# Optimization experiments

Hardware: AMD Instinct MI355X
Metric: run time of the kernel (lower is better)

## Reference

```python
import jax, jax.numpy as jnp
import numpy as np

N = 100000
H, C = 2, 16
EPS = 1e-16


def gatv2_conv(x, Wl, Wr, att, bias, src, dst, n):
    # x: [N, Fin]; Wl/Wr: [Fin, H*C]; att: [H, C]; bias: [H*C]
    xl = (x @ Wl).reshape(n, H, C)  # source-side transform
    xr = (x @ Wr).reshape(n, H, C)  # destination-side transform
    # per-edge GATv2 score: a^T LeakyReLU(xl_j + xr_i)
    z = jax.nn.leaky_relu(xl[src] + xr[dst], negative_slope=0.2)  # [E, H, C]
    e = jnp.einsum('ehc,hc->eh', z, att)  # [E, H]
    # softmax over incoming edges per destination node
    m = jax.ops.segment_max(e, dst, num_segments=n)  # [N, H]
    ex = jnp.exp(e - m[dst])
    s = jax.ops.segment_sum(ex, dst, num_segments=n)  # [N, H]
    alpha = ex / (s[dst] + EPS)  # [E, H]
    # scatter-add aggregation of weighted source features
    out = jax.ops.segment_sum(alpha[:, :, None] * xl[src], dst, num_segments=n)  # [N, H, C]
    return out.reshape(n, H * C) + bias


def setup_inputs() -> dict:
    key = jax.random.key(0)
    ks = jax.random.split(key, 12)
    F_in, n_cls, E = 1433, 7, 3200000
    x = jax.random.normal(ks[0], (N, F_in), dtype=jnp.float32)
    edge_index = jax.random.randint(ks[1], (2, E), 0, N, dtype=jnp.int64)
    sc = 0.05
    return {
        'x': x,
        'edge_index': edge_index,
        'Wl1': jax.random.normal(ks[2], (F_in, H * C), dtype=jnp.float32) * sc,
        'Wr1': jax.random.normal(ks[3], (F_in, H * C), dtype=jnp.float32) * sc,
        'a1': jax.random.normal(ks[4], (H, C), dtype=jnp.float32) * sc,
        'b1': jnp.zeros((H * C,), dtype=jnp.float32),
        'Wl2': jax.random.normal(ks[5], (H * C, H * C), dtype=jnp.float32) * sc,
        'Wr2': jax.random.normal(ks[6], (H * C, H * C), dtype=jnp.float32) * sc,
        'a2': jax.random.normal(ks[7], (H, C), dtype=jnp.float32) * sc,
        'b2': jnp.zeros((H * C,), dtype=jnp.float32),
        'fcW': jax.random.normal(ks[8], (H * C, n_cls), dtype=jnp.float32) * sc,
        'fcb': jnp.zeros((n_cls,), dtype=jnp.float32),
    }


def reference(x, edge_index, Wl1, Wr1, a1, b1, Wl2, Wr2, a2, b2, fcW, fcb):
    n = x.shape[0]
    loops = jnp.arange(n, dtype=edge_index.dtype)
    src = jnp.concatenate([edge_index[0], loops])  # add self-loops (PyG default)
    dst = jnp.concatenate([edge_index[1], loops])
    h = jax.nn.elu(gatv2_conv(x, Wl1, Wr1, a1, b1, src, dst, n))
    h = jax.nn.elu(gatv2_conv(h, Wl2, Wr2, a2, b2, src, dst, n))
    logits = h @ fcW + fcb
    return jax.nn.log_softmax(logits, axis=1)
```

## Files before the change

kernel.cpp:

```cpp
#include <hip/hip_runtime.h>
#include <hip/hip_bf16.h>
#include <cstddef>
#include <cstdint>

#define HC 32
#define NHEADS 2
#define CH 16
#define CAP 96

#define KK    1433
#define KFULL 1408
#define WTP   1440

typedef __bf16 bf16x8 __attribute__((ext_vector_type(8)));
typedef float  f32x4  __attribute__((ext_vector_type(4)));
typedef float  f32x4u __attribute__((ext_vector_type(4), aligned(4)));

#define BM 128

__global__ __launch_bounds__(256) void wprep(
    const float* __restrict__ Wl, const float* __restrict__ Wr,
    __bf16* __restrict__ Wt)
{
    int idx = blockIdx.x * 256 + threadIdx.x;
    if (idx >= 64 * WTP) return;
    int n = idx / WTP;
    int k = idx - n * WTP;
    float v = 0.f;
    if (k < KK) v = (n < HC) ? Wl[(size_t)k * HC + n]
                             : Wr[(size_t)k * HC + (n - HC)];
    Wt[idx] = (__bf16)v;
}

__global__ __launch_bounds__(256) void gemm_dual_mfma(
    const float* __restrict__ A, int N,
    const __bf16* __restrict__ Wt,
    float* __restrict__ XL, float* __restrict__ XR)
{
    const int tid  = threadIdx.x;
    const int lane = tid & 63;
    const int w    = tid >> 6;
    const int row0 = blockIdx.x * BM;
    const int frag_m = lane & 15;
    const int frag_k = lane >> 4;

    f32x4 acc[2][4];
    #pragma unroll
    for (int i = 0; i < 2; ++i)
        #pragma unroll
        for (int j = 0; j < 4; ++j) acc[i][j] = (f32x4){0.f, 0.f, 0.f, 0.f};

    int r0 = row0 + w * 32 + frag_m;
    int r1 = r0 + 16;
    int cr0 = (r0 < N) ? r0 : N - 1;
    int cr1 = (r1 < N) ? r1 : N - 1;
    const float* __restrict__ a0 = A + (size_t)cr0 * KK + frag_k * 8;
    const float* __restrict__ a1 = A + (size_t)cr1 * KK + frag_k * 8;
    const __bf16* __restrict__ wb = Wt + (size_t)frag_m * WTP + frag_k * 8;

    #pragma unroll 4
    for (int k0 = 0; k0 < KFULL; k0 += 32) {
        f32x4u u0 = *(const f32x4u*)(a0 + k0);
        f32x4u u1 = *(const f32x4u*)(a0 + k0 + 4);
        f32x4u v0 = *(const f32x4u*)(a1 + k0);
        f32x4u v1 = *(const f32x4u*)(a1 + k0 + 4);
        bf16x8 bfv[4];
        #pragma unroll
        for (int nt = 0; nt < 4; ++nt)
            bfv[nt] = *(const bf16x8*)(wb + (size_t)(nt * 16) * WTP + k0);
        bf16x8 af0, af1;
        #pragma unroll
        for (int j = 0; j < 4; ++j) {
            af0[j]     = (__bf16)u0[j];
            af0[j + 4] = (__bf16)u1[j];
            af1[j]     = (__bf16)v0[j];
            af1[j + 4] = (__bf16)v1[j];
        }
        #pragma unroll
        for (int nt = 0; nt < 4; ++nt) {
            acc[0][nt] = __builtin_amdgcn_mfma_f32_16x16x32_bf16(
                af0, bfv[nt], acc[0][nt], 0, 0, 0);
            acc[1][nt] = __builtin_amdgcn_mfma_f32_16x16x32_bf16(
                af1, bfv[nt], acc[1][nt], 0, 0, 0);
        }
    }

    {
        bf16x8 af0, af1, bfv[4];
        #pragma unroll
        for (int j = 0; j < 8; ++j) {
            int k = KFULL + frag_k * 8 + j;
            float x0 = (k < KK) ? a0[KFULL + j] : 0.f;
            float x1 = (k < KK) ? a1[KFULL + j] : 0.f;
            af0[j] = (__bf16)x0;
            af1[j] = (__bf16)x1;
        }
        #pragma unroll
        for (int nt = 0; nt < 4; ++nt)
            bfv[nt] = *(const bf16x8*)(wb + (size_t)(nt * 16) * WTP + KFULL);
        #pragma unroll
        for (int nt = 0; nt < 4; ++nt) {
            acc[0][nt] = __builtin_amdgcn_mfma_f32_16x16x32_bf16(
                af0, bfv[nt], acc[0][nt], 0, 0, 0);
            acc[1][nt] = __builtin_amdgcn_mfma_f32_16x16x32_bf16(
                af1, bfv[nt], acc[1][nt], 0, 0, 0);
        }
    }

    const int cl = lane & 15;
    const int rq = (lane >> 4) * 4;
    #pragma unroll
    for (int mt = 0; mt < 2; ++mt) {
        #pragma unroll
        for (int nt = 0; nt < 4; ++nt) {
            int col = nt * 16 + cl;
            float* dst = (col < HC) ? XL : XR;
            int c = (col < HC) ? col : (col - HC);
            #pragma unroll
            for (int r = 0; r < 4; ++r) {
                int grow = row0 + w * 32 + mt * 16 + rq + r;
                if (grow < N) dst[(size_t)grow * HC + c] = acc[mt][nt][r];
            }
        }
    }
}

__global__ __launch_bounds__(256) void gemm_dual(
    const float* __restrict__ A, int N, int K,
    const float* __restrict__ Wl, const float* __restrict__ Wr,
    float* __restrict__ XL, float* __restrict__ XR)
{
    __shared__ __align__(16) float As[64][33];
    __shared__ __align__(16) float Ws[32][68];
    const int tid = threadIdx.x;
    const int tx = tid & 15;
    const int ty = tid >> 4;
    const int row0 = blockIdx.x * 64;

    float acc[4][4];
    #pragma unroll
    for (int i = 0; i < 4; ++i)
        #pragma unroll
        for (int j = 0; j < 4; ++j) acc[i][j] = 0.f;

    for (int k0 = 0; k0 < K; k0 += 32) {
        #pragma unroll
        for (int i = 0; i < 8; ++i) {
            int idx = tid + i * 256;
            int r = idx >> 5;
            int kk = idx & 31;
            int gr = row0 + r, gk = k0 + kk;
            As[r][kk] = (gr < N && gk < K) ? A[(size_t)gr * K + gk] : 0.f;
        }
        #pragma unroll
        for (int i = 0; i < 8; ++i) {
            int idx = tid + i * 256;
            int kk = idx >> 6;
            int c = idx & 63;
            int gk = k0 + kk;
            float v = 0.f;
            if (gk < K) v = (c < HC) ? Wl[(size_t)gk * HC + c]
                                     : Wr[(size_t)gk * HC + (c - HC)];
            Ws[kk][c] = v;
        }
        __syncthreads();
        #pragma unroll
        for (int kk = 0; kk < 32; ++kk) {
            const float4 bv = *(const float4*)(&Ws[kk][tx * 4]);
            float av[4];
            #pragma unroll
            for (int i = 0; i < 4; ++i) av[i] = As[ty * 4 + i][kk];
            #pragma unroll
            for (int i = 0; i < 4; ++i) {
                acc[i][0] = fmaf(av[i], bv.x, acc[i][0]);
                acc[i][1] = fmaf(av[i], bv.y, acc[i][1]);
                acc[i][2] = fmaf(av[i], bv.z, acc[i][2]);
                acc[i][3] = fmaf(av[i], bv.w, acc[i][3]);
            }
        }
        __syncthreads();
    }
    #pragma unroll
    for (int i = 0; i < 4; ++i) {
        int gr = row0 + ty * 4 + i;
        if (gr < N) {
            float4 v = make_float4(acc[i][0], acc[i][1], acc[i][2], acc[i][3]);
            int c0 = tx * 4;
            if (c0 < HC) *(float4*)&XL[(size_t)gr * HC + c0] = v;
            else         *(float4*)&XR[(size_t)gr * HC + (c0 - HC)] = v;
        }
    }
}

__global__ __launch_bounds__(256) void scatter_fixed(
    const int* __restrict__ src, const int* __restrict__ dst,
    int E, int Etot, int* __restrict__ cnt, int* __restrict__ csr_src)
{
    int e = blockIdx.x * blockDim.x + threadIdx.x;
    if (e >= Etot) return;
    int si, di;
    if (e < E) { si = src[e]; di = dst[e]; }
    else       { si = e - E;  di = si; }
    int pos = atomicAdd(&cnt[di], 1);
    if (pos < CAP) csr_src[(size_t)di * CAP + pos] = si;
}

__global__ __launch_bounds__(256) void gather_pass(
    const float* __restrict__ xl, float* __restrict__ xr,
    const float* __restrict__ att, const int* __restrict__ cnt,
    const int* __restrict__ csr_src, const float* __restrict__ bias, int N)
{
    int d = (blockIdx.x * blockDim.x + threadIdx.x) >> 6;
    if (d >= N) return;
    const int lane = threadIdx.x & 63;
    const int c = lane & 31;
    const int eslot = lane >> 5;

    const float xrc  = xr[(size_t)d * HC + c];
    const float attc = att[c];
    const float bc   = bias[c];
    int deg = cnt[d]; if (deg > CAP) deg = CAP;
    const int* __restrict__ row = csr_src + (size_t)d * CAP;

    float accv = 0.f, den = 0.f;
    int p = eslot;
    for (; p + 6 < deg; p += 8) {
        int s0 = row[p], s1 = row[p + 2], s2 = row[p + 4], s3 = row[p + 6];
        float x0 = xl[(size_t)s0 * HC + c];
        float x1 = xl[(size_t)s1 * HC + c];
        float x2 = xl[(size_t)s2 * HC + c];
        float x3 = xl[(size_t)s3 * HC + c];
        float z0 = x0 + xrc; z0 = z0 > 0.f ? z0 : 0.2f * z0;
        float z1 = x1 + xrc; z1 = z1 > 0.f ? z1 : 0.2f * z1;
        float z2 = x2 + xrc; z2 = z2 > 0.f ? z2 : 0.2f * z2;
        float z3 = x3 + xrc; z3 = z3 > 0.f ? z3 : 0.2f * z3;
        float t0 = z0 * attc, t1 = z1 * attc, t2 = z2 * attc, t3 = z3 * attc;
        t0 += __shfl_xor(t0, 1); t1 += __shfl_xor(t1, 1);
        t2 += __shfl_xor(t2, 1); t3 += __shfl_xor(t3, 1);
        t0 += __shfl_xor(t0, 2); t1 += __shfl_xor(t1, 2);
        t2 += __shfl_xor(t2, 2); t3 += __shfl_xor(t3, 2);
        t0 += __shfl_xor(t0, 4); t1 += __shfl_xor(t1, 4);
        t2 += __shfl_xor(t2, 4); t3 += __shfl_xor(t3, 4);
        t0 += __shfl_xor(t0, 8); t1 += __shfl_xor(t1, 8);
        t2 += __shfl_xor(t2, 8); t3 += __shfl_xor(t3, 8);
        float e0 = __expf(t0), e1 = __expf(t1);
        float e2 = __expf(t2), e3 = __expf(t3);
        den += (e0 + e1) + (e2 + e3);
        accv = fmaf(e0, x0, accv);
        accv = fmaf(e1, x1, accv);
        accv = fmaf(e2, x2, accv);
        accv = fmaf(e3, x3, accv);
    }
    for (; p < deg; p += 2) {
        int sid = row[p];
        float x0 = xl[(size_t)sid * HC + c];
        float z = x0 + xrc;
        z = z > 0.f ? z : 0.2f * z;
        float t = z * attc;
        t += __shfl_xor(t, 1);
        t += __shfl_xor(t, 2);
        t += __shfl_xor(t, 4);
        t += __shfl_xor(t, 8);
        float ex = __expf(t);
        den += ex;
        accv = fmaf(ex, x0, accv);
    }
    accv += __shfl_xor(accv, 32);
    den  += __shfl_xor(den, 32);
    if (eslot == 0) {
        float v = accv / (den + 1e-16f) + bc;
        v = v > 0.f ? v : expm1f(v);
        xr[(size_t)d * HC + c] = v;
    }
}

__global__ __launch_bounds__(256) void fc_logsoftmax(
    const float* __restrict__ h, const float* __restrict__ W,
    const float* __restrict__ b, float* __restrict__ out, int N)
{
    int n = blockIdx.x * blockDim.x + threadIdx.x;
    if (n >= N) return;
    float hv[32];
    const float4* h4 = (const float4*)(h + (size_t)n * HC);
    #pragma unroll
    for (int j = 0; j < 8; ++j) {
        float4 t = h4[j];
        hv[j * 4 + 0] = t.x; hv[j * 4 + 1] = t.y;
        hv[j * 4 + 2] = t.z; hv[j * 4 + 3] = t.w;
    }
    float lg[7];
    #pragma unroll
    for (int c = 0; c < 7; ++c) lg[c] = b[c];
    #pragma unroll
    for (int k = 0; k < 32; ++k) {
        float hk = hv[k];
        #pragma unroll
        for (int c = 0; c < 7; ++c) lg[c] = fmaf(hk, W[k * 7 + c], lg[c]);
    }
    float m = lg[0];
    #pragma unroll
    for (int c = 1; c < 7; ++c) m = fmaxf(m, lg[c]);
    float sum = 0.f;
    #pragma unroll
    for (int c = 0; c < 7; ++c) sum += expf(lg[c] - m);
    float lse = m + logf(sum);
    #pragma unroll
    for (int c = 0; c < 7; ++c) out[(size_t)n * 7 + c] = lg[c] - lse;
}

extern "C" void kernel_launch(void* const* d_in, const int* in_sizes, int n_in,
                              void* d_out, int out_size, void* d_ws, size_t ws_size,
                              hipStream_t stream) {
    const float* x   = (const float*)d_in[0];
    const int*   ei  = (const int*)d_in[1];
    const float* Wl1 = (const float*)d_in[2];
    const float* Wr1 = (const float*)d_in[3];
    const float* a1  = (const float*)d_in[4];
    const float* b1  = (const float*)d_in[5];
    const float* Wl2 = (const float*)d_in[6];
    const float* Wr2 = (const float*)d_in[7];
    const float* a2  = (const float*)d_in[8];
    const float* b2  = (const float*)d_in[9];
    const float* fcW = (const float*)d_in[10];
    const float* fcb = (const float*)d_in[11];
    float* out = (float*)d_out;

    const int Fin  = 1433;
    const int N    = in_sizes[0] / Fin;
    const int E    = in_sizes[1] / 2;
    const int Etot = E + N;

    float*  xl      = (float*)d_ws;
    float*  xr      = xl + (size_t)N * HC;
    int*    cnt     = (int*)(xr + (size_t)N * HC);
    int*    csr_src = cnt + N;
    __bf16* Wt      = (__bf16*)(csr_src + (size_t)N * CAP);

    const int* srcp = ei;
    const int* dstp = ei + E;

    dim3 blk(256);
    dim3 gM((N + BM - 1) / BM);
    dim3 gN64((N + 63) / 64);
    dim3 gE((Etot + 255) / 256);
    dim3 gW((N * 64 + 255) / 256);
    dim3 gN((N + 255) / 256);
    dim3 gWp((64 * WTP + 255) / 256);

    wprep<<<gWp, blk, 0, stream>>>(Wl1, Wr1, Wt);
    hipMemsetAsync(cnt, 0, (size_t)N * sizeof(int), stream);
    scatter_fixed<<<gE, blk, 0, stream>>>(srcp, dstp, E, Etot, cnt, csr_src);

    gemm_dual_mfma<<<gM, blk, 0, stream>>>(x, N, Wt, xl, xr);
    gather_pass<<<gW, blk, 0, stream>>>(xl, xr, a1, cnt, csr_src, b1, N);
    gemm_dual<<<gN64, blk, 0, stream>>>(xr, N, HC, Wl2, Wr2, xl, xr);
    gather_pass<<<gW, blk, 0, stream>>>(xl, xr, a2, cnt, csr_src, b2, N);
    fc_logsoftmax<<<gN, blk, 0, stream>>>(xr, fcW, fcb, out, N);
}
```

Measured before the change: 1.343 ms.

## Stage A tiles into LDS via async global_load_lds with double buffering

The dual GEMM now streams its fp32 A tile into a double-buffered, XOR-swizzled shared-memory buffer using direct global-to-LDS loads, instead of each lane issuing unaligned 16-byte global loads. The next K-slice is prefetched while MFMAs run on the current one, synchronised with manual waitcnt and sched_barrier. The goal is to hide global memory latency and coalesce the reads of the large 1433-wide input. It relies on per-wave buffers and hand-written waitcnt counts, which are fragile if the instruction count or ordering changes.

```diff
diff --git a/kernel.cpp b/kernel.cpp
--- a/kernel.cpp
+++ b/kernel.cpp
@@ -10,11 +10,11 @@
 
 #define KK    1433
 #define KFULL 1408
+#define NT_K  44
 #define WTP   1440
 
 typedef __bf16 bf16x8 __attribute__((ext_vector_type(8)));
 typedef float  f32x4  __attribute__((ext_vector_type(4)));
-typedef float  f32x4u __attribute__((ext_vector_type(4), aligned(4)));
 
 #define BM 128
 
@@ -37,6 +37,7 @@
     const __bf16* __restrict__ Wt,
     float* __restrict__ XL, float* __restrict__ XR)
 {
+    __shared__ float Abuf[2][4096];
     const int tid  = threadIdx.x;
     const int lane = tid & 63;
     const int w    = tid >> 6;
@@ -50,39 +51,74 @@
         #pragma unroll
         for (int j = 0; j < 4; ++j) acc[i][j] = (f32x4){0.f, 0.f, 0.f, 0.f};
 
-    int r0 = row0 + w * 32 + frag_m;
-    int r1 = r0 + 16;
-    int cr0 = (r0 < N) ? r0 : N - 1;
-    int cr1 = (r1 < N) ? r1 : N - 1;
+    const int sr = lane >> 5;
+    const int sd = lane & 31;
+    const int fsw = (frag_m & 7) << 2;
+
+    const __bf16* __restrict__ wb = Wt + (size_t)frag_m * WTP + frag_k * 8;
+
+    int r0g = row0 + w * 32 + frag_m;
+    int r1g = r0g + 16;
+    int cr0 = (r0g < N) ? r0g : N - 1;
+    int cr1 = (r1g < N) ? r1g : N - 1;
     const float* __restrict__ a0 = A + (size_t)cr0 * KK + frag_k * 8;
     const float* __restrict__ a1 = A + (size_t)cr1 * KK + frag_k * 8;
-    const __bf16* __restrict__ wb = Wt + (size_t)frag_m * WTP + frag_k * 8;
-
-    #pragma unroll 4
-    for (int k0 = 0; k0 < KFULL; k0 += 32) {
-        f32x4u u0 = *(const f32x4u*)(a0 + k0);
-        f32x4u u1 = *(const f32x4u*)(a0 + k0 + 4);
-        f32x4u v0 = *(const f32x4u*)(a1 + k0);
-        f32x4u v1 = *(const f32x4u*)(a1 + k0 + 4);
+
+    auto stage = [&](int b, int k0) {
+        #pragma unroll
+        for (int i = 0; i < 16; ++i) {
+            int r  = 2 * i + sr;
+            int gr = row0 + w * 32 + r;
+            if (gr >= N) gr = N - 1;
+            int col = sd ^ ((r & 7) << 2);
+            const float* gsrc = A + (size_t)gr * KK + (k0 + col);
+            uint32_t* lbase = (uint32_t*)&Abuf[b][w * 1024 + i * 64];
+            __builtin_amdgcn_global_load_lds(
+                (const __attribute__((address_space(1))) uint32_t*)gsrc,
+                (__attribute__((address_space(3))) uint32_t*)lbase, 4, 0, 0);
+        }
+    };
+
+    auto computeA = [&](int b, const bf16x8* bfv) {
+        #pragma unroll
+        for (int mt = 0; mt < 2; ++mt) {
+            int r_l = mt * 16 + frag_m;
+            const float* rb = &Abuf[b][w * 1024 + r_l * 32];
+            f32x4 lo = *(const f32x4*)(rb + ((frag_k * 8) ^ fsw));
+            f32x4 hi = *(const f32x4*)(rb + ((frag_k * 8 + 4) ^ fsw));
+            bf16x8 af;
+            #pragma unroll
+            for (int j = 0; j < 4; ++j) {
+                af[j]     = (__bf16)lo[j];
+                af[j + 4] = (__bf16)hi[j];
+            }
+            #pragma unroll
+            for (int nt = 0; nt < 4; ++nt)
+                acc[mt][nt] = __builtin_amdgcn_mfma_f32_16x16x32_bf16(
+                    af, bfv[nt], acc[mt][nt], 0, 0, 0);
+        }
+    };
+
+    stage(0, 0);
+    for (int t = 0; t < NT_K - 1; ++t) {
+        asm volatile("s_waitcnt lgkmcnt(0)" ::: "memory");
+        stage((t + 1) & 1, (t + 1) * 32);
         bf16x8 bfv[4];
         #pragma unroll
         for (int nt = 0; nt < 4; ++nt)
-            bfv[nt] = *(const bf16x8*)(wb + (size_t)(nt * 16) * WTP + k0);
-        bf16x8 af0, af1;
-        #pragma unroll
-        for (int j = 0; j < 4; ++j) {
-            af0[j]     = (__bf16)u0[j];
-            af0[j + 4] = (__bf16)u1[j];
-            af1[j]     = (__bf16)v0[j];
-            af1[j + 4] = (__bf16)v1[j];
-        }
-        #pragma unroll
-        for (int nt = 0; nt < 4; ++nt) {
-            acc[0][nt] = __builtin_amdgcn_mfma_f32_16x16x32_bf16(
-                af0, bfv[nt], acc[0][nt], 0, 0, 0);
-            acc[1][nt] = __builtin_amdgcn_mfma_f32_16x16x32_bf16(
-                af1, bfv[nt], acc[1][nt], 0, 0, 0);
-        }
+            bfv[nt] = *(const bf16x8*)(wb + (size_t)(nt * 16) * WTP + t * 32);
+        asm volatile("s_waitcnt vmcnt(16)" ::: "memory");
+        __builtin_amdgcn_sched_barrier(0);
+        computeA(t & 1, bfv);
+    }
+    {
+        bf16x8 bfv[4];
+        #pragma unroll
+        for (int nt = 0; nt < 4; ++nt)
+            bfv[nt] = *(const bf16x8*)(wb + (size_t)(nt * 16) * WTP + (NT_K - 1) * 32);
+        asm volatile("s_waitcnt vmcnt(0)" ::: "memory");
+        __builtin_amdgcn_sched_barrier(0);
+        computeA((NT_K - 1) & 1, bfv);
     }
 
     {
```

Measured after the change: 1.284 ms. 4.4% less time.
